# Optimization experiments

Measured on AMD Instinct MI355X. Metric: run time of the kernel, lower is better.

## Reference

```python
import jax, jax.numpy as jnp
import numpy as np

N_NODES = 40000
N_EDGES = 640000
H = 128
N_REL2 = 474  # 2 * n_rel
BN_EPS = 1e-5


def setup_inputs() -> dict:
    key = jax.random.key(0)
    k1, k2, k3, k4, k5 = jax.random.split(key, 5)
    ent_emb = jax.random.normal(k1, (N_NODES, H), dtype=jnp.float32)
    rel_emb = jax.random.normal(k2, (N_REL2, H), dtype=jnp.float32)
    neigh_w = jax.random.normal(k3, (H, H), dtype=jnp.float32) * (1.0 / np.sqrt(H))
    bn_gamma = jnp.ones((H,), dtype=jnp.float32)
    bn_beta = jnp.zeros((H,), dtype=jnp.float32)
    rel_id = jax.random.randint(k4, (N_EDGES,), 0, N_REL2, dtype=jnp.int64)
    dst = jax.random.randint(k5, (N_EDGES,), 0, N_NODES, dtype=jnp.int64)
    return {"ent_emb": ent_emb, "rel_emb": rel_emb, "neigh_w": neigh_w,
            "bn_gamma": bn_gamma, "bn_beta": bn_beta, "rel_id": rel_id, "dst": dst}


def reference(ent_emb, rel_emb, neigh_w, bn_gamma, bn_beta, rel_id, dst):
    # per-edge relation embedding (gather)            [E, H]
    e = rel_emb[rel_id]
    # e_dot_v: edge emb dot destination node emb      [E]
    s = jnp.einsum('eh,eh->e', e, ent_emb[dst])
    # edge_softmax: softmax of s over edges grouped by destination node
    smax = jax.ops.segment_max(s, dst, num_segments=N_NODES)  # [N]
    ex = jnp.exp(s - smax[dst])
    denom = jax.ops.segment_sum(ex, dst, num_segments=N_NODES)  # [N]
    norm = ex / denom[dst]                                       # [E]
    # copy_e + sum: weighted scatter-sum of edge embeddings to dst nodes
    neigh = jax.ops.segment_sum(e * norm[:, None], dst, num_segments=N_NODES)  # [N, H]
    # dense update: mm + BatchNorm1d (training-mode batch stats) + tanh
    h = neigh @ neigh_w
    mean = jnp.mean(h, axis=0)
    var = jnp.var(h, axis=0)
    h = (h - mean) * jax.lax.rsqrt(var + BN_EPS) * bn_gamma + bn_beta
    return jnp.tanh(h)
```

## Files before the change

kernel.cpp:

```cpp
#include <hip/hip_runtime.h>

#define N_NODES 40000
#define N_EDGES 640000
#define HD 128
#define N_REL2 474
#define BN_EPS 1e-5f

typedef _Float16 half8 __attribute__((ext_vector_type(8)));
typedef float f32x4 __attribute__((ext_vector_type(4)));

__global__ __launch_bounds__(256) void k_cnt(
        const int* __restrict__ dst, const int* __restrict__ rel_id,
        unsigned* __restrict__ cntT) {
    int e = blockIdx.x * 256 + threadIdx.x;
    if (e < N_EDGES) {
        int d = dst[e], r = rel_id[e];
        int nb = d >> 5, lrow = d & 31;
        atomicAdd(&cntT[(size_t)(nb * 480 + r) * 4 + (lrow >> 3)], 1u << ((lrow & 7) * 4));
    }
}

__global__ __launch_bounds__(128) void k_rw(
        const float* __restrict__ R, const float* __restrict__ W,
        _Float16* __restrict__ R_hl, _Float16* __restrict__ RWT) {
    __shared__ float row[HD];
    int r = blockIdx.x, c = threadIdx.x;
    float rv = (r < N_REL2) ? R[(size_t)r * HD + c] : 0.f;
    row[c] = rv;
    _Float16 hh = (_Float16)rv;
    R_hl[r * 256 + c] = hh;
    R_hl[r * 256 + 128 + c] = (_Float16)(rv - (float)hh);
    __syncthreads();
    float acc = 0.f;
    #pragma unroll 8
    for (int k = 0; k < HD; ++k) acc += row[k] * W[(size_t)k * HD + c];
    _Float16 ah = (_Float16)acc;
    RWT[c * 960 + r] = ah;
    RWT[c * 960 + 480 + r] = (_Float16)(acc - (float)ah);
}

__global__ __launch_bounds__(256) void k_fat(
        const float* __restrict__ ent, const _Float16* __restrict__ R_hl,
        const _Float16* __restrict__ RWT, const unsigned* __restrict__ cntT,
        float* __restrict__ h) {
    __shared__ __align__(16) unsigned char lds[79872];
    _Float16* As  = (_Float16*)lds;
    unsigned* cl  = (unsigned*)(lds + 31232);
    float*    mh  = (float*)(lds + 40832);
    float*    lsu = (float*)(lds + 41088);
    char*     Bst = (char*)(lds + 41472);

    int t = threadIdx.x, w = t >> 6, l = t & 63, lr = l & 15, lk = l >> 4;
    int nb = blockIdx.x;
    int rh = w & 1, ch = w >> 1;
    int node = nb * 32 + rh * 16 + lr;

    const unsigned* cg = cntT + (size_t)nb * 1920;
    for (int i = t; i < 1920; i += 256)
        cl[(i >> 2) * 5 + (i & 3)] = cg[i];

    f32x4 acc[15];
    #pragma unroll
    for (int i = 0; i < 15; ++i) acc[i] = (f32x4){0.f, 0.f, 0.f, 0.f};

    for (int kf = 0; kf < 4; ++kf) {
        const float* ep = ent + (size_t)node * HD + kf * 32 + lk * 8;
        float4 v0 = *(const float4*)ep;
        float4 v1 = *(const float4*)(ep + 4);
        float vv[8] = {v0.x, v0.y, v0.z, v0.w, v1.x, v1.y, v1.z, v1.w};
        half8 ah, al;
        #pragma unroll
        for (int j = 0; j < 8; ++j) {
            _Float16 hh = (_Float16)vv[j];
            ah[j] = hh;
            al[j] = (_Float16)(vv[j] - (float)hh);
        }
        for (int i = t; i < 1920; i += 256) {
            int rel = i >> 2, seg = i & 3;
            *(float4*)(Bst + rel * 80 + seg * 16) =
                *(const float4*)(R_hl + (size_t)rel * 256 + kf * 32 + seg * 8);
        }
        __syncthreads();
        #pragma unroll
        for (int tl = 0; tl < 15; ++tl) {
            const char* bp = Bst + (ch * 240 + tl * 16 + lr) * 80 + lk * 16;
            half8 bh = *(const half8*)bp;
            acc[tl] = __builtin_amdgcn_mfma_f32_16x16x32_f16(ah, bh, acc[tl], 0, 0, 0);
            acc[tl] = __builtin_amdgcn_mfma_f32_16x16x32_f16(al, bh, acc[tl], 0, 0, 0);
        }
        __syncthreads();
        for (int i = t; i < 1920; i += 256) {
            int rel = i >> 2, seg = i & 3;
            *(float4*)(Bst + rel * 80 + seg * 16) =
                *(const float4*)(R_hl + (size_t)rel * 256 + 128 + kf * 32 + seg * 8);
        }
        __syncthreads();
        #pragma unroll
        for (int tl = 0; tl < 15; ++tl) {
            const char* bp = Bst + (ch * 240 + tl * 16 + lr) * 80 + lk * 16;
            half8 bl = *(const half8*)bp;
            acc[tl] = __builtin_amdgcn_mfma_f32_16x16x32_f16(ah, bl, acc[tl], 0, 0, 0);
        }
        __syncthreads();
    }

    unsigned cw[15];
    int cwsel = rh * 2 + (lk >> 1);
    #pragma unroll
    for (int tl = 0; tl < 15; ++tl)
        cw[tl] = cl[(ch * 240 + tl * 16 + lr) * 5 + cwsel];

    float m[4];
    #pragma unroll
    for (int reg = 0; reg < 4; ++reg) {
        int shift = ((lk & 1) * 4 + reg) * 4;
        float mm = -INFINITY;
        #pragma unroll
        for (int tl = 0; tl < 15; ++tl)
            if ((cw[tl] >> shift) & 15u) mm = fmaxf(mm, acc[tl][reg]);
        #pragma unroll
        for (int msk = 1; msk <= 8; msk <<= 1)
            mm = fmaxf(mm, __shfl_xor(mm, msk, 64));
        if (lr == 0) mh[ch * 32 + rh * 16 + lk * 4 + reg] = mm;
        m[reg] = mm;
    }
    __syncthreads();
    #pragma unroll
    for (int reg = 0; reg < 4; ++reg) {
        int row = rh * 16 + lk * 4 + reg;
        m[reg] = fmaxf(mh[row], mh[32 + row]);
    }

    float ps[4] = {0.f, 0.f, 0.f, 0.f};
    #pragma unroll
    for (int tl = 0; tl < 15; ++tl) {
        int col = ch * 240 + tl * 16 + lr;
        #pragma unroll
        for (int reg = 0; reg < 4; ++reg) {
            int shift = ((lk & 1) * 4 + reg) * 4;
            unsigned nib = (cw[tl] >> shift) & 15u;
            float a = 0.f;
            if (nib) a = (float)nib * __expf(acc[tl][reg] - m[reg]);
            ps[reg] += a;
            As[(rh * 16 + lk * 4 + reg) * 488 + col] = (_Float16)a;
        }
    }
    #pragma unroll
    for (int reg = 0; reg < 4; ++reg) {
        #pragma unroll
        for (int msk = 1; msk <= 8; msk <<= 1)
            ps[reg] += __shfl_xor(ps[reg], msk, 64);
        if (lr == 0) lsu[ch * 32 + rh * 16 + lk * 4 + reg] = ps[reg];
    }
    __syncthreads();

    int rh2 = w & 1, ch2 = w >> 1;
    f32x4 a2[4];
    #pragma unroll
    for (int i = 0; i < 4; ++i) a2[i] = (f32x4){0.f, 0.f, 0.f, 0.f};
    for (int kf2 = 0; kf2 < 15; ++kf2) {
        for (int i = t; i < 1024; i += 256) {
            int plane = i >> 9, j = i & 511, col = j >> 2, seg = j & 3;
            *(float4*)(Bst + plane * 10240 + col * 80 + seg * 16) =
                *(const float4*)(RWT + (size_t)col * 960 + plane * 480 + kf2 * 32 + seg * 8);
        }
        __syncthreads();
        half8 af = *(const half8*)((const char*)As + (rh2 * 16 + lr) * 976 + kf2 * 64 + lk * 16);
        #pragma unroll
        for (int t2 = 0; t2 < 4; ++t2) {
            const char* bp = Bst + (ch2 * 64 + t2 * 16 + lr) * 80 + lk * 16;
            half8 bh = *(const half8*)bp;
            half8 bl = *(const half8*)(bp + 10240);
            a2[t2] = __builtin_amdgcn_mfma_f32_16x16x32_f16(af, bh, a2[t2], 0, 0, 0);
            a2[t2] = __builtin_amdgcn_mfma_f32_16x16x32_f16(af, bl, a2[t2], 0, 0, 0);
        }
        __syncthreads();
    }

    #pragma unroll
    for (int reg = 0; reg < 4; ++reg) {
        int row = rh2 * 16 + lk * 4 + reg;
        float lv = lsu[row] + lsu[32 + row];
        float invl = (lv > 0.f) ? 1.f / lv : 0.f;
        #pragma unroll
        for (int t2 = 0; t2 < 4; ++t2)
            h[((size_t)nb * 32 + row) * HD + ch2 * 64 + t2 * 16 + lr] = a2[t2][reg] * invl;
    }
}

__global__ __launch_bounds__(256) void k_stats(
        const float* __restrict__ Hout, float* __restrict__ colsum,
        float* __restrict__ colsumsq) {
    __shared__ float ls[256], lq[256];
    int t = threadIdx.x;
    int c = t & 127, half = t >> 7;
    int rbase = blockIdx.x * 64;
    float sum = 0.f, sq = 0.f;
    #pragma unroll 4
    for (int i = 0; i < 32; ++i) {
        int r = rbase + half + i * 2;
        float v = Hout[(size_t)r * HD + c];
        sum += v;
        sq += v * v;
    }
    ls[t] = sum;
    lq[t] = sq;
    __syncthreads();
    if (t < 128) {
        sum = ls[t] + ls[t + 128];
        sq = lq[t] + lq[t + 128];
        atomicAdd(colsum + c, sum);
        atomicAdd(colsumsq + c, sq);
    }
}

__global__ __launch_bounds__(256) void k_apply(
        float* __restrict__ Hout, const float* __restrict__ colsum,
        const float* __restrict__ colsumsq, const float* __restrict__ gamma,
        const float* __restrict__ beta) {
    int idx = blockIdx.x * 256 + threadIdx.x;
    if (idx >= N_NODES * HD / 4) return;
    int c0 = (idx * 4) & 127;
    float4 hv4 = ((const float4*)Hout)[idx];
    const float inv = 1.f / (float)N_NODES;
    float hv[4] = {hv4.x, hv4.y, hv4.z, hv4.w};
    float o[4];
    #pragma unroll
    for (int j = 0; j < 4; ++j) {
        int c = c0 + j;
        float mean = colsum[c] * inv;
        float var = colsumsq[c] * inv - mean * mean;
        float rstd = rsqrtf(var + BN_EPS);
        float x = (hv[j] - mean) * rstd * gamma[c] + beta[c];
        o[j] = 1.f - 2.f / (__expf(2.f * x) + 1.f);
    }
    ((float4*)Hout)[idx] = make_float4(o[0], o[1], o[2], o[3]);
}

extern "C" void kernel_launch(void* const* d_in, const int* in_sizes, int n_in,
                              void* d_out, int out_size, void* d_ws, size_t ws_size,
                              hipStream_t stream) {
    const float* ent_emb  = (const float*)d_in[0];
    const float* rel_emb  = (const float*)d_in[1];
    const float* neigh_w  = (const float*)d_in[2];
    const float* bn_gamma = (const float*)d_in[3];
    const float* bn_beta  = (const float*)d_in[4];
    const int*   rel_id   = (const int*)d_in[5];
    const int*   dst      = (const int*)d_in[6];
    float* out = (float*)d_out;

    unsigned* cntT   = (unsigned*)d_ws;
    float*    colsum = (float*)d_ws + 2400000;
    float*    colsumsq = colsum + 128;
    _Float16* R_hl   = (_Float16*)((float*)d_ws + 2400256);
    _Float16* RWT    = (_Float16*)((float*)d_ws + 2461696);

    hipMemsetAsync(d_ws, 0, (size_t)2400256 * 4, stream);

    k_cnt<<<(N_EDGES + 255) / 256, 256, 0, stream>>>(dst, rel_id, cntT);
    k_rw<<<480, 128, 0, stream>>>(rel_emb, neigh_w, R_hl, RWT);
    k_fat<<<N_NODES / 32, 256, 0, stream>>>(ent_emb, R_hl, RWT, cntT, out);
    k_stats<<<N_NODES / 64, 256, 0, stream>>>(out, colsum, colsumsq);
    k_apply<<<N_NODES * HD / 4 / 256, 256, 0, stream>>>(out, colsum, colsumsq, bn_gamma, bn_beta);
}
```

Before: 176.3 us.

## Read B operands directly from global/L2 instead of LDS staging in k_fat

```diff
diff --git a/kernel.cpp b/kernel.cpp
--- a/kernel.cpp
+++ b/kernel.cpp
@@ -39,16 +39,15 @@
     RWT[c * 960 + 480 + r] = (_Float16)(acc - (float)ah);
 }
 
-__global__ __launch_bounds__(256) void k_fat(
+__global__ __launch_bounds__(256, 3) void k_fat(
         const float* __restrict__ ent, const _Float16* __restrict__ R_hl,
         const _Float16* __restrict__ RWT, const unsigned* __restrict__ cntT,
         float* __restrict__ h) {
-    __shared__ __align__(16) unsigned char lds[79872];
+    __shared__ __align__(16) unsigned char lds[41344];
     _Float16* As  = (_Float16*)lds;
     unsigned* cl  = (unsigned*)(lds + 31232);
     float*    mh  = (float*)(lds + 40832);
     float*    lsu = (float*)(lds + 41088);
-    char*     Bst = (char*)(lds + 41472);
 
     int t = threadIdx.x, w = t >> 6, l = t & 63, lr = l & 15, lk = l >> 4;
     int nb = blockIdx.x;
@@ -75,34 +74,17 @@
             ah[j] = hh;
             al[j] = (_Float16)(vv[j] - (float)hh);
         }
-        for (int i = t; i < 1920; i += 256) {
-            int rel = i >> 2, seg = i & 3;
-            *(float4*)(Bst + rel * 80 + seg * 16) =
-                *(const float4*)(R_hl + (size_t)rel * 256 + kf * 32 + seg * 8);
-        }
-        __syncthreads();
         #pragma unroll
         for (int tl = 0; tl < 15; ++tl) {
-            const char* bp = Bst + (ch * 240 + tl * 16 + lr) * 80 + lk * 16;
+            const _Float16* bp = R_hl + (size_t)(ch * 240 + tl * 16 + lr) * 256 + kf * 32 + lk * 8;
             half8 bh = *(const half8*)bp;
+            half8 bl = *(const half8*)(bp + 128);
             acc[tl] = __builtin_amdgcn_mfma_f32_16x16x32_f16(ah, bh, acc[tl], 0, 0, 0);
             acc[tl] = __builtin_amdgcn_mfma_f32_16x16x32_f16(al, bh, acc[tl], 0, 0, 0);
-        }
-        __syncthreads();
-        for (int i = t; i < 1920; i += 256) {
-            int rel = i >> 2, seg = i & 3;
-            *(float4*)(Bst + rel * 80 + seg * 16) =
-                *(const float4*)(R_hl + (size_t)rel * 256 + 128 + kf * 32 + seg * 8);
-        }
-        __syncthreads();
-        #pragma unroll
-        for (int tl = 0; tl < 15; ++tl) {
-            const char* bp = Bst + (ch * 240 + tl * 16 + lr) * 80 + lk * 16;
-            half8 bl = *(const half8*)bp;
             acc[tl] = __builtin_amdgcn_mfma_f32_16x16x32_f16(ah, bl, acc[tl], 0, 0, 0);
         }
-        __syncthreads();
-    }
+    }
+    __syncthreads();
 
     unsigned cw[15];
     int cwsel = rh * 2 + (lk >> 1);
@@ -122,7 +104,6 @@
         for (int msk = 1; msk <= 8; msk <<= 1)
             mm = fmaxf(mm, __shfl_xor(mm, msk, 64));
         if (lr == 0) mh[ch * 32 + rh * 16 + lk * 4 + reg] = mm;
-        m[reg] = mm;
     }
     __syncthreads();
     #pragma unroll
@@ -159,22 +140,16 @@
     #pragma unroll
     for (int i = 0; i < 4; ++i) a2[i] = (f32x4){0.f, 0.f, 0.f, 0.f};
     for (int kf2 = 0; kf2 < 15; ++kf2) {
-        for (int i = t; i < 1024; i += 256) {
-            int plane = i >> 9, j = i & 511, col = j >> 2, seg = j & 3;
-            *(float4*)(Bst + plane * 10240 + col * 80 + seg * 16) =
-                *(const float4*)(RWT + (size_t)col * 960 + plane * 480 + kf2 * 32 + seg * 8);
-        }
-        __syncthreads();
         half8 af = *(const half8*)((const char*)As + (rh2 * 16 + lr) * 976 + kf2 * 64 + lk * 16);
         #pragma unroll
         for (int t2 = 0; t2 < 4; ++t2) {
-            const char* bp = Bst + (ch2 * 64 + t2 * 16 + lr) * 80 + lk * 16;
+            int col2 = ch2 * 64 + t2 * 16 + lr;
+            const _Float16* bp = RWT + (size_t)col2 * 960 + kf2 * 32 + lk * 8;
             half8 bh = *(const half8*)bp;
-            half8 bl = *(const half8*)(bp + 10240);
+            half8 bl = *(const half8*)(bp + 480);
             a2[t2] = __builtin_amdgcn_mfma_f32_16x16x32_f16(af, bh, a2[t2], 0, 0, 0);
             a2[t2] = __builtin_amdgcn_mfma_f32_16x16x32_f16(af, bl, a2[t2], 0, 0, 0);
         }
-        __syncthreads();
     }
 
     #pragma unroll
```

Result: slower. 221.6 us (+25.7%).
